# Kernel optimization log

Measured on AMD Instinct MI355X. Metric: run time of the kernel, lower is better.

## Reference

```python
import jax, jax.numpy as jnp
import numpy as np
from jax import lax

D_INNER = 1024
D_STATE = 16
DT_RANK = 32


def conv2d(x, w, b, pad=1):
    y = lax.conv_general_dilated(x, w, (1, 1), [(pad, pad), (pad, pad)],
                                 dimension_numbers=('NCHW', 'OIHW', 'NCHW'))
    return y + b[None, :, None, None]


def maxpool2(x):
    return lax.reduce_window(x, -jnp.inf, lax.max, (1, 1, 2, 2), (1, 1, 2, 2), 'VALID')


def layer_norm(x, w, b, eps=1e-5):
    m = x.mean(-1, keepdims=True)
    v = ((x - m) ** 2).mean(-1, keepdims=True)
    return (x - m) * lax.rsqrt(v + eps) * w + b


def cblock(h, w1, b1, w2, b2):
    return jax.nn.relu(conv2d(jax.nn.relu(conv2d(h, w1, b1)), w2, b2))


def up2(d, w, b):
    # ConvTranspose2d(kernel=2, stride=2): each input pixel -> 2x2 output block
    Bn, Ci, H, W = d.shape
    y = jnp.einsum('bcij,copq->boipjq', d, w).reshape(Bn, w.shape[1], 2 * H, 2 * W)
    return y + b[None, :, None, None]


def eblock(e, d, upw, upb, w1, b1, w2, b2):
    d = up2(d, upw, upb)
    dy = e.shape[2] - d.shape[2]
    dx = e.shape[3] - d.shape[3]
    e = e[:, :, dy // 2:e.shape[2] - dy // 2, dx // 2:e.shape[3] - dx // 2]
    return cblock(jnp.concatenate([e, d], 1), w1, b1, w2, b2)


def mamba(hs, inW, cw, cb, xpW, dtW, dtB, Alog, Dp, outW):
    # standard Mamba-1 mixer: in_proj -> causal depthwise conv -> selective scan -> gate -> out_proj
    Bn, L, _ = hs.shape
    xz = jnp.einsum('bld,ed->ble', hs, inW)                       # [B,L,2*d_inner]
    xi, z = xz[..., :D_INNER], xz[..., D_INNER:]
    xc = lax.conv_general_dilated(xi.transpose(0, 2, 1), cw[:, None, :], (1,), [(3, 0)],
                                  dimension_numbers=('NCH', 'OIH', 'NCH'),
                                  feature_group_count=D_INNER)    # causal, len L
    xc = jax.nn.silu(xc + cb[None, :, None]).transpose(0, 2, 1)   # [B,L,d_inner]
    xdbl = jnp.einsum('bld,ed->ble', xc, xpW)                     # [B,L,dt_rank+2*d_state]
    dt = jax.nn.softplus(jnp.einsum('blr,dr->bld', xdbl[..., :DT_RANK], dtW) + dtB)
    Bs = xdbl[..., DT_RANK:DT_RANK + D_STATE]
    Cs = xdbl[..., DT_RANK + D_STATE:]
    A = -jnp.exp(Alog)                                            # [d_inner,d_state]
    dA = jnp.exp(dt[..., None] * A)                               # [B,L,d_inner,d_state]
    dBu = (dt * xc)[..., None] * Bs[:, :, None, :]

    def step(h, inp):
        dA_t, dBu_t, C_t = inp
        h = dA_t * h + dBu_t
        return h, jnp.einsum('bdn,bn->bd', h, C_t)

    h0 = jnp.zeros((Bn, D_INNER, D_STATE), hs.dtype)
    _, ys = lax.scan(step, h0, (dA.transpose(1, 0, 2, 3), dBu.transpose(1, 0, 2, 3), Cs.transpose(1, 0, 2)))
    y = ys.transpose(1, 0, 2) + Dp * xc
    return jnp.einsum('ble,de->bld', y * jax.nn.silu(z), outW)


def setup_inputs() -> dict:
    key = jax.random.key(0)
    ks = iter(jax.random.split(key, 80))

    def w(shape, fan_in):
        return jax.random.normal(next(ks), shape, jnp.float32) * np.float32(np.sqrt(2.0 / fan_in))

    H = W = 128
    fy = np.fft.fftfreq(H)
    fx = np.fft.fftfreq(W)
    r = np.sqrt(fy[:, None] ** 2 + fx[None, :] ** 2)
    r = r / r.max()
    bands = [(0.0, 0.15), (0.15, 0.35), (0.35, 1.0001)]
    freq_masks = jnp.asarray(np.stack([((r >= lo) & (r < hi)).astype(np.float32) for lo, hi in bands]))

    d = {}
    d['x'] = jax.random.normal(next(ks), (2, 1, H, W), jnp.float32)
    d['freq_masks'] = freq_masks
    for ci, co, n in [(3, 64, 'e1'), (64, 128, 'e2'), (128, 256, 'e3'), (256, 512, 'e4')]:
        d[n + 'w1'] = w((co, ci, 3, 3), ci * 9)
        d[n + 'b1'] = jnp.zeros((co,), jnp.float32)
        d[n + 'w2'] = w((co, co, 3, 3), co * 9)
        d[n + 'b2'] = jnp.zeros((co,), jnp.float32)
    d['cls_token'] = jnp.zeros((1, 1, 512), jnp.float32)
    d['norm_w'] = jnp.ones((24, 512), jnp.float32)
    d['norm_b'] = jnp.zeros((24, 512), jnp.float32)
    d['in_proj_w'] = w((24, 2048, 512), 512)
    d['conv1d_w'] = w((24, 1024, 4), 4)
    d['conv1d_b'] = jnp.zeros((24, 1024), jnp.float32)
    d['x_proj_w'] = w((24, 64, 1024), 1024)
    d['dt_w'] = w((24, 1024, 32), 32)
    d['dt_b'] = jnp.full((24, 1024), float(np.log(np.expm1(0.01))), jnp.float32)
    d['A_log'] = jnp.broadcast_to(jnp.log(jnp.arange(1, 17, dtype=jnp.float32)), (24, 1024, 16)) + 0.0
    d['D_ssm'] = jnp.ones((24, 1024), jnp.float32)
    d['out_proj_w'] = w((24, 512, 1024), 1024)
    for n, ci, co, cc in [('d4', 512, 256, 768), ('d3', 256, 128, 384), ('d2', 128, 64, 192), ('d1', 64, 32, 96)]:
        d[n + 'up_w'] = w((ci, co, 2, 2), ci * 4)
        d[n + 'up_b'] = jnp.zeros((co,), jnp.float32)
        d[n + 'w1'] = w((co, cc, 3, 3), cc * 9)
        d[n + 'b1'] = jnp.zeros((co,), jnp.float32)
        d[n + 'w2'] = w((co, co, 3, 3), co * 9)
        d[n + 'b2'] = jnp.zeros((co,), jnp.float32)
    d['final_w'] = w((4, 32, 1, 1), 32)
    d['final_b'] = jnp.zeros((4,), jnp.float32)
    return d


def reference(x, freq_masks, e1w1, e1b1, e1w2, e1b2, e2w1, e2b1, e2w2, e2b2,
              e3w1, e3b1, e3w2, e3b2, e4w1, e4b1, e4w2, e4b2, cls_token,
              norm_w, norm_b, in_proj_w, conv1d_w, conv1d_b, x_proj_w, dt_w, dt_b,
              A_log, D_ssm, out_proj_w,
              d4up_w, d4up_b, d4w1, d4b1, d4w2, d4b2,
              d3up_w, d3up_b, d3w1, d3b1, d3w2, d3b2,
              d2up_w, d2up_b, d2w1, d2b1, d2w2, d2b2,
              d1up_w, d1up_b, d1w1, d1b1, d1w2, d1b2,
              final_w, final_b):
    # DCT/FFT frequency split: [B,1,H,W] -> [B,3,H,W]
    xf = jnp.fft.fft2(x)
    x_freq = jnp.real(jnp.fft.ifft2(xf * freq_masks[None]))

    e1 = cblock(x_freq, e1w1, e1b1, e1w2, e1b2); p1 = maxpool2(e1)
    e2 = cblock(p1, e2w1, e2b1, e2w2, e2b2); p2 = maxpool2(e2)
    e3 = cblock(p2, e3w1, e3b1, e3w2, e3b2); p3 = maxpool2(e3)
    e4 = cblock(p3, e4w1, e4b1, e4w2, e4b2); p4 = maxpool2(e4)   # [B,512,H/16,W/16]

    Bn, _, Hs, Ws = p4.shape
    seq = p4.reshape(Bn, 512, Hs * Ws).transpose(0, 2, 1)
    tok = jnp.concatenate([jnp.broadcast_to(cls_token, (Bn, 1, 512)), seq], 1)

    params = (norm_w, norm_b, in_proj_w, conv1d_w, conv1d_b, x_proj_w, dt_w, dt_b, A_log, D_ssm, out_proj_w)

    def layer(carry, p):
        hidden, residual = carry
        nw, nb, inW, cw, cb, xpW, dtW, dtB, Alog, Dp, outW = p
        residual = residual + hidden   # first block: residual starts == hidden (faithful)
        hs = layer_norm(residual, nw, nb)
        hs = mamba(hs, inW, cw, cb, xpW, dtW, dtB, Alog, Dp, outW)
        return (hs, residual), None

    (hidden, _), _ = lax.scan(layer, (tok, tok), params)

    xsp = hidden[:, 1:, :].transpose(0, 2, 1).reshape(Bn, 512, Hs, Ws)

    d4 = eblock(e4, xsp, d4up_w, d4up_b, d4w1, d4b1, d4w2, d4b2)
    d3 = eblock(e3, d4, d3up_w, d3up_b, d3w1, d3b1, d3w2, d3b2)
    d2 = eblock(e2, d3, d2up_w, d2up_b, d2w1, d2b1, d2w2, d2b2)
    d1 = eblock(e1, d2, d1up_w, d1up_b, d1w1, d1b1, d1w2, d1b2)

    out = conv2d(d1, final_w, final_b, pad=0)
    out = jax.image.resize(out, (out.shape[0], out.shape[1], out.shape[2] * 16, out.shape[3] * 16), 'bilinear')
    return out
```

## Files before the change

kernel.cpp:

```cpp
#include <hip/hip_runtime.h>
#include <math.h>

#define PI_F 3.14159265358979323846f
typedef _Float16 f16;
typedef __attribute__((ext_vector_type(8))) _Float16 f16x8;
typedef __attribute__((ext_vector_type(4))) float f32x4;

__device__ __forceinline__ float siluf(float x){ return x / (1.f + expf(-x)); }
__device__ __forceinline__ float softplusf(float x){ return fmaxf(x,0.f) + log1pf(expf(-fabsf(x))); }
__device__ __forceinline__ void f2hl(float v, f16& hi, f16& lo){
  hi = (f16)v;
  lo = (f16)(v - (float)hi);
}

__global__ void k_dft_rows(const float* __restrict__ x, float* __restrict__ Tre, float* __restrict__ Tim){
  int v = threadIdx.x; int y = blockIdx.x; int b = blockIdx.y;
  __shared__ float cs[128], sn[128];
  float ang = -2.f*PI_F*(float)v/128.f;
  cs[v]=cosf(ang); sn[v]=sinf(ang);
  __syncthreads();
  const float* row = x + (b*128+y)*128;
  float re=0.f, im=0.f;
  for(int n=0;n<128;n++){ float xv=row[n]; int ph=(v*n)&127; re=fmaf(xv,cs[ph],re); im=fmaf(xv,sn[ph],im); }
  int o=(b*128+y)*128+v; Tre[o]=re; Tim[o]=im;
}
__global__ void k_dft_cols(const float* __restrict__ Tre, const float* __restrict__ Tim,
                           float* __restrict__ Fre, float* __restrict__ Fim){
  int v=threadIdx.x; int u=blockIdx.x; int b=blockIdx.y;
  __shared__ float cs[128], sn[128];
  float ang=-2.f*PI_F*(float)v/128.f; cs[v]=cosf(ang); sn[v]=sinf(ang);
  __syncthreads();
  float re=0.f,im=0.f;
  for(int y=0;y<128;y++){
    int ph=(u*y)&127; float c=cs[ph], s=sn[ph];
    int o=(b*128+y)*128+v;
    float tr=Tre[o], ti=Tim[o];
    re += tr*c - ti*s; im += tr*s + ti*c;
  }
  int o=(b*128+u)*128+v; Fre[o]=re; Fim[o]=im;
}
__global__ void k_idft_cols(const float* __restrict__ Fre,const float* __restrict__ Fim,
                            const float* __restrict__ mask, float* __restrict__ Gre,float* __restrict__ Gim){
  int v=threadIdx.x; int y=blockIdx.x; int m=blockIdx.y; int b=blockIdx.z;
  __shared__ float cs[128], sn[128];
  float ang=-2.f*PI_F*(float)v/128.f; cs[v]=cosf(ang); sn[v]=sinf(ang);
  __syncthreads();
  float re=0.f,im=0.f;
  for(int u=0;u<128;u++){
    int ph=(u*y)&127; float c=cs[ph], s=sn[ph];
    float w = mask[(m*128+u)*128+v];
    int o=(b*128+u)*128+v;
    float fr=Fre[o]*w, fi=Fim[o]*w;
    re += fr*c + fi*s;
    im += fi*c - fr*s;
  }
  int o=((b*3+m)*128+y)*128+v;
  Gre[o]=re*(1.f/128.f); Gim[o]=im*(1.f/128.f);
}
__global__ void k_idft_rows(const float* __restrict__ Gre,const float* __restrict__ Gim, float* __restrict__ xf){
  int xc=threadIdx.x; int y=blockIdx.x; int m=blockIdx.y; int b=blockIdx.z;
  __shared__ float cs[128], sn[128];
  float ang=-2.f*PI_F*(float)xc/128.f; cs[xc]=cosf(ang); sn[xc]=sinf(ang);
  __syncthreads();
  float re=0.f;
  const float* gr=Gre+((b*3+m)*128+y)*128;
  const float* gi=Gim+((b*3+m)*128+y)*128;
  for(int v=0;v<128;v++){
    int ph=(v*xc)&127;
    re += gr[v]*cs[ph] + gi[v]*sn[ph];
  }
  xf[((b*3+m)*128+y)*128+xc] = re*(1.f/128.f);
}

#define NWD 20
struct WAll {
  const float* src[NWD];
  int N[NWD], Kp[NWD], up[NWD], ci[NWD], cip[NWD];
  int cum[NWD+1];
};
__global__ void k_wcvt_all(WAll d, int total, f16* __restrict__ bh, f16* __restrict__ bl){
  int gid = blockIdx.x*256 + threadIdx.x;
  if (gid >= total) return;
  int li = gid; const float* src = d.src[0];
  int N=d.N[0], Kp=d.Kp[0], up=d.up[0], Ci=d.ci[0], cip=d.cip[0];
  #pragma unroll
  for (int j=1;j<NWD;j++){
    if (gid >= d.cum[j]){
      li = gid - d.cum[j]; src=d.src[j]; N=d.N[j];Kp=d.Kp[j];up=d.up[j];Ci=d.ci[j];cip=d.cip[j];
    }
  }
  int n = li / Kp, k = li - n*Kp;
  float v = 0.f;
  if (up){
    int o = n>>2, p=(n>>1)&1, q=n&1;
    if (k < Ci) v = src[(((size_t)k*up + o)*2 + p)*2 + q];
  } else {
    int tap = k / cip, cc = k - tap*cip;
    if (n < N && cc < Ci) v = src[((size_t)n*Ci + cc)*9 + tap];
  }
  f16 h,l; f2hl(v,h,l);
  bh[gid]=h; bl[gid]=l;
}

__global__ void k_im2col(const float* __restrict__ in1, int C1,
                         int H, int W, int wsh, int hwsh, int K, int Kp,
                         f16* __restrict__ Ah, f16* __restrict__ Al){
  int k = blockIdx.x*256 + threadIdx.x;
  int lm = blockIdx.y;
  if (k >= Kp) return;
  float val = 0.f;
  if (k < K){
    int m = lm;
    int b = m >> hwsh;
    int hw = m & ((1<<hwsh)-1);
    int y = hw >> wsh;
    int x = hw & (W-1);
    val = in1[(((size_t)b*C1 + k)*H + y)*W + x];
  }
  f16 h,l; f2hl(val,h,l);
  Ah[(size_t)lm*Kp + k] = h; Al[(size_t)lm*Kp + k] = l;
}

__global__ void k_im2col32(const float* __restrict__ in1, int C1,
                           const float* __restrict__ in2, int C2,
                           int H, int W, int wsh, int hwsh, int K,
                           float* __restrict__ A){
  int k = blockIdx.x*256 + threadIdx.x;
  int m = blockIdx.y;
  if (k >= K) return;
  int ci = k/9; int tt = k - ci*9;
  int dy = tt/3 - 1, dx = tt - (tt/3)*3 - 1;
  int b = m >> hwsh;
  int hw = m & ((1<<hwsh)-1);
  int y = (hw >> wsh) + dy;
  int x = (hw & (W-1)) + dx;
  float val = 0.f;
  if (y >= 0 && y < H && x >= 0 && x < W){
    val = (ci < C1) ? in1[(((size_t)b*C1 + ci)*H + y)*W + x]
                    : in2[(((size_t)b*C2 + (ci-C1))*H + y)*W + x];
  }
  A[(size_t)m*K + k] = val;
}

#define GLLDS(gp, ls) __builtin_amdgcn_global_load_lds( \
    (const __attribute__((address_space(1))) void*)(gp), \
    (__attribute__((address_space(3))) void*)(ls), 16, 0, 0)

template<int NL>
__global__ __launch_bounds__(256) void k_conv_ig(
    const float* __restrict__ in1, int C1, const float* __restrict__ in2, int C2,
    const f16* __restrict__ Wh, const f16* __restrict__ Wl,
    const float* __restrict__ bias, float* __restrict__ out,
    int Co, int H, int W, int wsh, int hwsh, int Cip, int civ)
{
  __shared__ __align__(16) float smI[2*6464];
  __shared__ __align__(16) f16 smW[3*2*2048];
  const int HW = 1<<hwsh;
  const int tw = (W<64)?W:64;
  const int twsh = (wsh<6)?wsh:6;
  const int R = 64>>twsh;
  const int RT = R+2, TWD = tw+2;
  const int nspat = RT*TWD;
  const int CS = ((nspat+3)&~3)+2;
  const int total = nspat*32;
  const int nslab = Cip>>5;
  const int nsteps = 9*nslab;
  const int Kp = 9*Cip;

  int bn = blockIdx.y*64;
  int bm = blockIdx.x*64;
  int t = threadIdx.x;
  int lane = t&63, wv = t>>6;
  int wr = wv>>1, wc = wv&1;

  int b  = bm >> hwsh;
  int hw0 = bm & (HW-1);
  int y0 = hw0 >> wsh;
  int x0 = hw0 & (W-1);

  float bv[2][4];
  {
    int cb = bn + wr*32 + (lane>>4)*4;
    #pragma unroll
    for (int ri=0;ri<2;ri++)
      #pragma unroll
      for (int r=0;r<4;r++){
        int co = cb + ri*16 + r;
        bv[ri][r] = bias[co < Co ? co : Co-1];
      }
    asm volatile("s_waitcnt vmcnt(0)" ::: "memory");
  }

  int goff[NL], loff[NL];
  {
    int ci = 0, s = t;
    if (s >= nspat){ s -= nspat; ci++; }
    if (s >= nspat){ s -= nspat; ci++; }
    #pragma unroll
    for (int j=0;j<NL;j++){
      int rr_=0, sx=s;
      #pragma unroll
      for (int q=0;q<5;q++){ if (sx>=TWD){ sx-=TWD; rr_++; } }
      int gy = y0 - 1 + rr_;
      int gx = x0 - 1 + sx;
      int idx = t + j*256;
      bool intile = (idx < total);
      bool ok = intile && (ci < civ) && (gy>=0) && (gy<H) && (gx>=0) && (gx<W);
      goff[j] = ok ? (ci*HW + gy*W + gx) : -1;
      loff[j] = intile ? (ci*CS + rr_*TWD + sx) : -1;
      s += 256;
      if (s >= nspat){ s -= nspat; ci++; }
      if (s >= nspat){ s -= nspat; ci++; }
      if (s >= nspat){ s -= nspat; ci++; }
    }
  }

  int rr = lane >> 2;
  int cg = (lane & 3) ^ ((lane >> 3) & 3);
  size_t gW = (size_t)(bn + wv*16 + rr)*Kp + cg*8;
  int lb = wv*512;
  auto stage = [&](int bfi, int k0){
    GLLDS(Wh + gW + k0, &smW[(bfi*2+0)*2048 + lb]);
    GLLDS(Wl + gW + k0, &smW[(bfi*2+1)*2048 + lb]);
  };

  int rA = lane & 15, c = lane >> 4;
  int RW = wr*32 + rA; int sW = (RW>>1)&3;
  int offW = RW*32 + 8*(c ^ sW);
  int lp0 = wc*32 + rA, lp1 = lp0 + 16;
  int sid0 = ((lp0>>twsh)+1)*TWD + (lp0 & (tw-1)) + 1;
  int sid1 = ((lp1>>twsh)+1)*TWD + (lp1 & (tw-1)) + 1;
  int cbase = c*8*CS;
  int csj[8];
  #pragma unroll
  for (int j=0;j<8;j++) csj[j] = j*CS;

  auto srcptr = [&](int sl) -> const float* {
    int cbeg = sl*32;
    return (cbeg < C1) ? in1 + ((size_t)(b*C1 + cbeg))*HW
                       : in2 + ((size_t)(b*C2 + (cbeg - C1)))*HW;
  };

  float rin[NL];
  {
    const float* sp = srcptr(0);
    #pragma unroll
    for (int j=0;j<NL;j++) rin[j] = sp[goff[j] < 0 ? 0 : goff[j]];
  }
  stage(0, 0);
  stage(1, Cip);
  stage(2, 2*Cip);
  asm volatile("s_waitcnt vmcnt(6)" ::: "memory");
  #pragma unroll
  for (int j=0;j<NL;j++) if (loff[j] >= 0) smI[loff[j]] = (goff[j] < 0) ? 0.f : rin[j];
  asm volatile("s_waitcnt lgkmcnt(0)" ::: "memory");
  __builtin_amdgcn_s_barrier();
  asm volatile("" ::: "memory");
  if (nslab > 1){
    const float* sp = srcptr(1);
    #pragma unroll
    for (int j=0;j<NL;j++) rin[j] = sp[goff[j] < 0 ? 0 : goff[j]];
  }

  f32x4 zz = {0.f,0.f,0.f,0.f};
  f32x4 acc[2][2];
  acc[0][0]=zz; acc[0][1]=zz; acc[1][0]=zz; acc[1][1]=zz;

  int tcur = 0, scur = 0;
  int stp_t3 = 3, stp_s3 = 0;
  int bfi = 0;

  for (int step = 0; step < nsteps; ++step){
    if (tcur == 0 && step > 0){
      asm volatile("s_waitcnt vmcnt(6)" ::: "memory");
      int wb = (scur & 1)*6464;
      #pragma unroll
      for (int j=0;j<NL;j++) if (loff[j] >= 0) smI[wb + loff[j]] = (goff[j] < 0) ? 0.f : rin[j];
      asm volatile("s_waitcnt lgkmcnt(0)" ::: "memory");
      __builtin_amdgcn_s_barrier();
      asm volatile("" ::: "memory");
      if (scur + 1 < nslab){
        const float* sp = srcptr(scur+1);
        #pragma unroll
        for (int j=0;j<NL;j++) rin[j] = sp[goff[j] < 0 ? 0 : goff[j]];
      }
    }
    if (tcur < 3 && (scur + 1 < nslab)){
      if constexpr (NL == 25) asm volatile("s_waitcnt vmcnt(29)" ::: "memory");
      else if constexpr (NL == 17) asm volatile("s_waitcnt vmcnt(21)" ::: "memory");
      else asm volatile("s_waitcnt vmcnt(18)" ::: "memory");
    } else {
      asm volatile("s_waitcnt vmcnt(4)" ::: "memory");
    }
    __builtin_amdgcn_s_barrier();
    asm volatile("" ::: "memory");

    const f16* bW = &smW[bfi*4096];
    f16x8 w0h = *(const f16x8*)&bW[offW];
    f16x8 w1h = *(const f16x8*)&bW[offW + 512];
    f16x8 w0l = *(const f16x8*)&bW[2048 + offW];
    f16x8 w1l = *(const f16x8*)&bW[2048 + offW + 512];

    int t3v = (tcur >= 6) ? 2 : ((tcur >= 3) ? 1 : 0);
    int doff = (t3v - 1)*TWD + (tcur - 3*t3v) - 1;
    int ib = (scur & 1)*6464 + cbase;
    f16x8 p0h, p0l, p1h, p1l;
    #pragma unroll
    for (int j=0;j<8;j++){
      float v0 = smI[ib + csj[j] + sid0 + doff];
      float v1 = smI[ib + csj[j] + sid1 + doff];
      f16 h0 = (f16)v0; p0h[j] = h0; p0l[j] = (f16)(v0 - (float)h0);
      f16 h1 = (f16)v1; p1h[j] = h1; p1l[j] = (f16)(v1 - (float)h1);
    }
    acc[0][0] = __builtin_amdgcn_mfma_f32_16x16x32_f16(w0h, p0h, acc[0][0], 0,0,0);
    acc[0][1] = __builtin_amdgcn_mfma_f32_16x16x32_f16(w0h, p1h, acc[0][1], 0,0,0);
    acc[1][0] = __builtin_amdgcn_mfma_f32_16x16x32_f16(w1h, p0h, acc[1][0], 0,0,0);
    acc[1][1] = __builtin_amdgcn_mfma_f32_16x16x32_f16(w1h, p1h, acc[1][1], 0,0,0);
    acc[0][0] = __builtin_amdgcn_mfma_f32_16x16x32_f16(w0h, p0l, acc[0][0], 0,0,0);
    acc[0][1] = __builtin_amdgcn_mfma_f32_16x16x32_f16(w0h, p1l, acc[0][1], 0,0,0);
    acc[1][0] = __builtin_amdgcn_mfma_f32_16x16x32_f16(w1h, p0l, acc[1][0], 0,0,0);
    acc[1][1] = __builtin_amdgcn_mfma_f32_16x16x32_f16(w1h, p1l, acc[1][1], 0,0,0);
    acc[0][0] = __builtin_amdgcn_mfma_f32_16x16x32_f16(w0l, p0h, acc[0][0], 0,0,0);
    acc[0][1] = __builtin_amdgcn_mfma_f32_16x16x32_f16(w0l, p1h, acc[0][1], 0,0,0);
    acc[1][0] = __builtin_amdgcn_mfma_f32_16x16x32_f16(w1l, p0h, acc[1][0], 0,0,0);
    acc[1][1] = __builtin_amdgcn_mfma_f32_16x16x32_f16(w1l, p1h, acc[1][1], 0,0,0);

    __builtin_amdgcn_s_barrier();
    asm volatile("" ::: "memory");
    int k0 = (stp_s3 < nslab) ? (stp_t3*Cip + stp_s3*32) : 0;
    stage(bfi, k0);
    if (++stp_t3 == 9){ stp_t3 = 0; stp_s3++; }
    bfi = (bfi == 2) ? 0 : bfi + 1;
    if (++tcur == 9){ tcur = 0; scur++; }
  }

  #pragma unroll
  for (int ri=0;ri<2;ri++)
  #pragma unroll
  for (int fc=0;fc<2;fc++)
  #pragma unroll
  for (int r=0;r<4;r++){
    int co = bn + wr*32 + ri*16 + (lane>>4)*4 + r;
    int pm = bm + wc*32 + fc*16 + (lane&15);
    if (co < Co){
      float v = acc[ri][fc][r] + bv[ri][r];
      v = fmaxf(v, 0.f);
      int hw = pm & (HW-1);
      out[((size_t)b*Co + co)*HW + hw] = v;
    }
  }
}

__global__ void k_creduce(const float* __restrict__ part, const float* __restrict__ bias,
                          float* __restrict__ out, int M, int Np, int msh, int cosh, int hwsh, int S){
  int i = blockIdx.x*256 + threadIdx.x;
  int Co = 1<<cosh;
  if (i >= M*Co) return;
  int co = i >> msh, m = i & (M-1);
  float v = bias[co];
  for (int s=0;s<S;s++) v += part[((size_t)s*M + m)*Np + co];
  v = fmaxf(v, 0.f);
  int HW = 1<<hwsh;
  int b = m >> hwsh, hw = m & (HW-1);
  out[((size_t)b*Co + co)*HW + hw] = v;
}

__global__ __launch_bounds__(256) void k_gemm_hl(
    const f16* __restrict__ Wh, const f16* __restrict__ Wl,
    const f16* __restrict__ Ph, const f16* __restrict__ Pl,
    const float* __restrict__ bias, float* __restrict__ out,
    int N, int Kp, int wsh, int hwsh, int Co)
{
  __shared__ __align__(16) f16 sm[3*4*2048];
  int bn = blockIdx.y*64;
  int bm = blockIdx.x*64;
  int t = threadIdx.x;
  int lane = t & 63, wv = t >> 6;
  int wr = wv >> 1, wc = wv & 1;

  float bv[2][4];
  {
    int cb = bn + wr*32 + (lane>>4)*4;
    #pragma unroll
    for (int ri=0;ri<2;ri++)
      #pragma unroll
      for (int r=0;r<4;r++){
        int co = cb + ri*16 + r;
        int idx = co>>2, lim = N>>2;
// ... 108 lines not shown
  int RP0 = wc*32 + rA;  int swzP = RP0 & 7;
  int cw0 = ((2*c)   ^ swzW)*4;
  int cw1 = ((2*c+1) ^ swzW)*4;
  int pc0 = ((2*c)   ^ swzP)*4;
  int pc1 = ((2*c+1) ^ swzP)*4;

  f32x4 zz = {0.f,0.f,0.f,0.f};
  f32x4 acc[2][2];
  acc[0][0]=zz; acc[0][1]=zz; acc[1][0]=zz; acc[1][1]=zz;

  auto stage = [&](int bfi, int kk){
    GLLDS(Wf + gWoff + kk,                  &smW[bfi*2048 + wv*512]);
    GLLDS(Wf + gWoff + kk + 8*(size_t)ldaW, &smW[bfi*2048 + wv*512 + 256]);
    GLLDS(Pf + gPoff + kk,                  &smP[bfi*2048 + wv*512]);
    GLLDS(Pf + gPoff + kk + 8*(size_t)ldaP, &smP[bfi*2048 + wv*512 + 256]);
  };

  int nt = KS >> 5;
  stage(0, 0);
  stage(1, (nt>1)?32:0);
  stage(2, (nt>2)?64:0);

  for (int tt = 0; tt < nt; ++tt){
    asm volatile("s_waitcnt vmcnt(8)" ::: "memory");
    __builtin_amdgcn_s_barrier();
    asm volatile("" ::: "memory");
    int bfi = tt % 3;
    const float* bW = &smW[bfi*2048];
    const float* bP = &smP[bfi*2048];
    f32x4 a0 = *(const f32x4*)&bW[RW0*32 + cw0];
    f32x4 a1 = *(const f32x4*)&bW[RW0*32 + cw1];
    f32x4 a2 = *(const f32x4*)&bW[RW0*32 + 512 + cw0];
    f32x4 a3 = *(const f32x4*)&bW[RW0*32 + 512 + cw1];
    f32x4 b0 = *(const f32x4*)&bP[RP0*32 + pc0];
    f32x4 b1 = *(const f32x4*)&bP[RP0*32 + pc1];
    f32x4 b2 = *(const f32x4*)&bP[RP0*32 + 512 + pc0];
    f32x4 b3 = *(const f32x4*)&bP[RP0*32 + 512 + pc1];
    f16x8 w0h, w0l, w1h, w1l, p0h, p0l, p1h, p1l;
    #pragma unroll
    for (int j=0;j<4;j++){
      f16 h;
      h=(f16)a0[j]; w0h[j]=h;   w0l[j]  =(f16)(a0[j]-(float)h);
      h=(f16)a1[j]; w0h[4+j]=h; w0l[4+j]=(f16)(a1[j]-(float)h);
      h=(f16)a2[j]; w1h[j]=h;   w1l[j]  =(f16)(a2[j]-(float)h);
      h=(f16)a3[j]; w1h[4+j]=h; w1l[4+j]=(f16)(a3[j]-(float)h);
      h=(f16)b0[j]; p0h[j]=h;   p0l[j]  =(f16)(b0[j]-(float)h);
      h=(f16)b1[j]; p0h[4+j]=h; p0l[4+j]=(f16)(b1[j]-(float)h);
      h=(f16)b2[j]; p1h[j]=h;   p1l[j]  =(f16)(b2[j]-(float)h);
      h=(f16)b3[j]; p1h[4+j]=h; p1l[4+j]=(f16)(b3[j]-(float)h);
    }
    acc[0][0] = __builtin_amdgcn_mfma_f32_16x16x32_f16(w0h, p0h, acc[0][0], 0,0,0);
    acc[0][1] = __builtin_amdgcn_mfma_f32_16x16x32_f16(w0h, p1h, acc[0][1], 0,0,0);
    acc[1][0] = __builtin_amdgcn_mfma_f32_16x16x32_f16(w1h, p0h, acc[1][0], 0,0,0);
    acc[1][1] = __builtin_amdgcn_mfma_f32_16x16x32_f16(w1h, p1h, acc[1][1], 0,0,0);
    acc[0][0] = __builtin_amdgcn_mfma_f32_16x16x32_f16(w0h, p0l, acc[0][0], 0,0,0);
    acc[0][1] = __builtin_amdgcn_mfma_f32_16x16x32_f16(w0h, p1l, acc[0][1], 0,0,0);
    acc[1][0] = __builtin_amdgcn_mfma_f32_16x16x32_f16(w1h, p0l, acc[1][0], 0,0,0);
    acc[1][1] = __builtin_amdgcn_mfma_f32_16x16x32_f16(w1h, p1l, acc[1][1], 0,0,0);
    acc[0][0] = __builtin_amdgcn_mfma_f32_16x16x32_f16(w0l, p0h, acc[0][0], 0,0,0);
    acc[0][1] = __builtin_amdgcn_mfma_f32_16x16x32_f16(w0l, p1h, acc[0][1], 0,0,0);
    acc[1][0] = __builtin_amdgcn_mfma_f32_16x16x32_f16(w1l, p0h, acc[1][0], 0,0,0);
    acc[1][1] = __builtin_amdgcn_mfma_f32_16x16x32_f16(w1l, p1h, acc[1][1], 0,0,0);
    __builtin_amdgcn_s_barrier();
    asm volatile("" ::: "memory");
    int kn = (tt+3 < nt) ? (tt+3)*32 : 0;
    stage(bfi, kn);
  }

  #pragma unroll
  for (int ri=0;ri<2;ri++)
  #pragma unroll
  for (int fc=0;fc<2;fc++)
  #pragma unroll
  for (int r=0;r<4;r++){
    int co = bn + wr*32 + ri*16 + (lane>>4)*4 + r;
    int m  = bm + wc*32 + fc*16 + (lane&15);
    if (m < Mreal)
      out[((size_t)blockIdx.z*sliceStride + m)*ldc + co] = acc[ri][fc][r];
  }
}

__global__ __launch_bounds__(256) void k_dt(
    const float* __restrict__ xdp, const float* __restrict__ dtW,
    const float* __restrict__ dtB, float* __restrict__ dtb)
{
  __shared__ float smP[64*36];
  __shared__ float smW[64*36];
  int bn = blockIdx.x*64;
  int bm = blockIdx.y*64;
  int t = threadIdx.x, lane = t&63, wv = t>>6, wr = wv>>1, wc = wv&1;
  {
    int row = t>>2, c0 = (t&3)*8;
    #pragma unroll
    for (int j=0;j<8;j++){
      int cc = c0+j;
      float pv = 0.f;
      #pragma unroll
      for (int s=0;s<4;s++) pv += xdp[((size_t)(s*192) + bm+row)*64 + cc];
      smP[row*36 + cc] = pv;
      smW[row*36 + cc] = dtW[(size_t)(bn+row)*32 + cc];
    }
  }
  __syncthreads();
  int rA = lane&15, c = lane>>4;
  int c8 = c*8;
  f32x4 a0 = *(const f32x4*)&smW[(wr*32+rA)*36 + c8];
  f32x4 a1 = *(const f32x4*)&smW[(wr*32+rA)*36 + c8+4];
  f32x4 a2 = *(const f32x4*)&smW[(wr*32+16+rA)*36 + c8];
  f32x4 a3 = *(const f32x4*)&smW[(wr*32+16+rA)*36 + c8+4];
  f32x4 b0 = *(const f32x4*)&smP[(wc*32+rA)*36 + c8];
  f32x4 b1 = *(const f32x4*)&smP[(wc*32+rA)*36 + c8+4];
  f32x4 b2 = *(const f32x4*)&smP[(wc*32+16+rA)*36 + c8];
  f32x4 b3 = *(const f32x4*)&smP[(wc*32+16+rA)*36 + c8+4];
  f16x8 w0h, w0l, w1h, w1l, p0h, p0l, p1h, p1l;
  #pragma unroll
  for (int j=0;j<4;j++){
    f16 h;
    h=(f16)a0[j]; w0h[j]=h;   w0l[j]  =(f16)(a0[j]-(float)h);
    h=(f16)a1[j]; w0h[4+j]=h; w0l[4+j]=(f16)(a1[j]-(float)h);
    h=(f16)a2[j]; w1h[j]=h;   w1l[j]  =(f16)(a2[j]-(float)h);
    h=(f16)a3[j]; w1h[4+j]=h; w1l[4+j]=(f16)(a3[j]-(float)h);
    h=(f16)b0[j]; p0h[j]=h;   p0l[j]  =(f16)(b0[j]-(float)h);
    h=(f16)b1[j]; p0h[4+j]=h; p0l[4+j]=(f16)(b1[j]-(float)h);
    h=(f16)b2[j]; p1h[j]=h;   p1l[j]  =(f16)(b2[j]-(float)h);
    h=(f16)b3[j]; p1h[4+j]=h; p1l[4+j]=(f16)(b3[j]-(float)h);
  }
  f32x4 zz = {0.f,0.f,0.f,0.f};
  f32x4 acc[2][2];
  acc[0][0]=zz; acc[0][1]=zz; acc[1][0]=zz; acc[1][1]=zz;
  acc[0][0] = __builtin_amdgcn_mfma_f32_16x16x32_f16(w0h, p0h, acc[0][0], 0,0,0);
  acc[0][1] = __builtin_amdgcn_mfma_f32_16x16x32_f16(w0h, p1h, acc[0][1], 0,0,0);
  acc[1][0] = __builtin_amdgcn_mfma_f32_16x16x32_f16(w1h, p0h, acc[1][0], 0,0,0);
  acc[1][1] = __builtin_amdgcn_mfma_f32_16x16x32_f16(w1h, p1h, acc[1][1], 0,0,0);
  acc[0][0] = __builtin_amdgcn_mfma_f32_16x16x32_f16(w0h, p0l, acc[0][0], 0,0,0);
  acc[0][1] = __builtin_amdgcn_mfma_f32_16x16x32_f16(w0h, p1l, acc[0][1], 0,0,0);
  acc[1][0] = __builtin_amdgcn_mfma_f32_16x16x32_f16(w1h, p0l, acc[1][0], 0,0,0);
  acc[1][1] = __builtin_amdgcn_mfma_f32_16x16x32_f16(w1h, p1l, acc[1][1], 0,0,0);
  acc[0][0] = __builtin_amdgcn_mfma_f32_16x16x32_f16(w0l, p0h, acc[0][0], 0,0,0);
  acc[0][1] = __builtin_amdgcn_mfma_f32_16x16x32_f16(w0l, p1h, acc[0][1], 0,0,0);
  acc[1][0] = __builtin_amdgcn_mfma_f32_16x16x32_f16(w1l, p0h, acc[1][0], 0,0,0);
  acc[1][1] = __builtin_amdgcn_mfma_f32_16x16x32_f16(w1l, p1h, acc[1][1], 0,0,0);
  #pragma unroll
  for (int ri=0;ri<2;ri++)
  #pragma unroll
  for (int fc=0;fc<2;fc++)
  #pragma unroll
  for (int r=0;r<4;r++){
    int co = bn + wr*32 + ri*16 + (lane>>4)*4 + r;
    int m  = bm + wc*32 + fc*16 + (lane&15);
    if (m < 130)
      dtb[(size_t)m*1024 + co] = softplusf(acc[ri][fc][r] + dtB[co]);
  }
}

__global__ void k_maxpool2(const float* __restrict__ in, float* __restrict__ out, int BC, int H, int W){
  int Ho=H/2, Wo=W/2;
  int idx = blockIdx.x*blockDim.x + threadIdx.x;
  if (idx >= BC*Ho*Wo) return;
  int xo = idx % Wo; int yo = (idx / Wo) % Ho; int c = idx / (Wo*Ho);
  const float* p = in + ((size_t)c*H + 2*yo)*W + 2*xo;
  out[idx] = fmaxf(fmaxf(p[0],p[1]), fmaxf(p[W],p[W+1]));
}

__global__ void k_build_tok(const float* __restrict__ p4, const float* __restrict__ cls,
                            float* __restrict__ hidp, float* __restrict__ residual){
  int idx = blockIdx.x*blockDim.x+threadIdx.x;
  if (idx >= 2*65*512) return;
  int d = idx % 512; int l = (idx/512)%65; int b = idx/(512*65);
  float v = (l==0) ? cls[d] : p4[((size_t)b*512+d)*64 + (l-1)];
  int row = b*65 + l;
  residual[(size_t)row*512 + d] = v;
  hidp[(size_t)row*512 + d] = v;
  #pragma unroll
  for (int s=1;s<8;s++) hidp[((size_t)(s*192) + row)*512 + d] = 0.f;
}

__global__ void k_add_ln(float* __restrict__ residual, const float* __restrict__ hidp,
                         const float* __restrict__ nw, const float* __restrict__ nb,
                         float* __restrict__ hs){
  int row = blockIdx.x;
  int t = threadIdx.x;
  __shared__ float red[256];
  size_t base = (size_t)row*512;
  float h0 = 0.f, h1 = 0.f;
  #pragma unroll
  for (int s=0;s<8;s++){
    h0 += hidp[((size_t)(s*192) + row)*512 + t];
    h1 += hidp[((size_t)(s*192) + row)*512 + 256 + t];
  }
  float v0 = residual[base + t]       + h0;
  float v1 = residual[base + 256 + t] + h1;
  residual[base+t]=v0; residual[base+256+t]=v1;
  red[t]=v0+v1; __syncthreads();
  for(int o=128;o>0;o>>=1){ if(t<o) red[t]+=red[t+o]; __syncthreads(); }
  float mean = red[0]/512.f; __syncthreads();
  float d0=v0-mean, d1=v1-mean;
  red[t]=d0*d0+d1*d1; __syncthreads();
  for(int o=128;o>0;o>>=1){ if(t<o) red[t]+=red[t+o]; __syncthreads(); }
  float rstd = rsqrtf(red[0]/512.f + 1e-5f);
  hs[base+t]     = d0*rstd*nw[t]     + nb[t];
  hs[base+256+t] = d1*rstd*nw[256+t] + nb[256+t];
}

__global__ void k_conv1d_silu(const float* __restrict__ xzp, const float* __restrict__ cw,
                              const float* __restrict__ cb, float* __restrict__ xc){
  int d = blockIdx.x*blockDim.x + threadIdx.x;
  int l = blockIdx.y, b = blockIdx.z;
  if (d>=1024) return;
  float acc = cb[d];
  #pragma unroll
  for(int k=0;k<4;k++){
    int lp = l-3+k;
    if (lp>=0){
      size_t r = (size_t)(b*65+lp);
      float xzv = xzp[r*2048 + d] + xzp[(r + 192)*2048 + d];
      acc = fmaf(xzv, cw[d*4+k], acc);
    }
  }
  xc[((size_t)(b*65+l))*1024 + d] = siluf(acc);
}

__global__ void k_scan(const float* __restrict__ dt, const float* __restrict__ xc,
                       const float* __restrict__ xdp, const float* __restrict__ xzp,
                       const float* __restrict__ Alog, const float* __restrict__ Dp,
                       float* __restrict__ gt){
  int gid = blockIdx.x*blockDim.x + threadIdx.x;
  if (gid >= 2*1024*16) return;
  int n = gid & 15;
  int d = (gid >> 4) & 1023;
  int b = gid >> 14;
  float A = -expf(Alog[d*16+n]);
  float Dv = Dp[d];
  float h = 0.f;
  for (int l=0;l<65;l++){
    size_t r = (size_t)(b*65+l);
    float dtv = dt[r*1024+d];
    float xcv = xc[r*1024+d];
    float Bn = 0.f, Cn = 0.f;
    #pragma unroll
    for (int s=0;s<4;s++){
      Bn += xdp[((size_t)(s*192) + r)*64 + 32 + n];
      Cn += xdp[((size_t)(s*192) + r)*64 + 48 + n];
    }
    h = fmaf(expf(dtv*A), h, dtv*xcv*Bn);
    float y = h*Cn;
    y += __shfl_xor(y, 1); y += __shfl_xor(y, 2);
    y += __shfl_xor(y, 4); y += __shfl_xor(y, 8);
    if (n==0){
      float zv = xzp[r*2048 + 1024 + d] + xzp[(r + 192)*2048 + 1024 + d];
      gt[r*1024+d] = (y + Dv*xcv) * siluf(zv);
    }
  }
}

__global__ void k_xsp(const float* __restrict__ hidp, float* __restrict__ xsp){
  int idx = blockIdx.x*blockDim.x+threadIdx.x;
  if (idx>=2*512*64) return;
  int j = idx & 63; int c = (idx>>6)&511; int b = idx>>15;
  int row = b*65 + 1 + j;
  float v = 0.f;
  #pragma unroll
  for (int s=0;s<8;s++) v += hidp[((size_t)(s*192) + row)*512 + c];
  xsp[idx] = v;
}

__global__ void k_conv1x1(const float* __restrict__ in, const float* __restrict__ w,
                          const float* __restrict__ bias, float* __restrict__ out){
  int hw = blockIdx.x*blockDim.x+threadIdx.x; if (hw>=128*128) return;
  int o = blockIdx.y, b = blockIdx.z;
  float acc = bias[o];
  #pragma unroll
  for(int c=0;c<32;c++) acc = fmaf(in[((size_t)(b*32+c))*16384 + hw], w[o*32+c], acc);
  out[((size_t)(b*4+o))*16384 + hw] = acc;
}

__global__ void k_resize16(const float* __restrict__ in, float* __restrict__ out){
  size_t idx = (size_t)blockIdx.x*blockDim.x + threadIdx.x;
  if (idx >= (size_t)2*4*2048*2048) return;
  int x = idx & 2047; int y = (int)((idx>>11)&2047); int c = (int)(idx>>22);
  float sx = ((float)x+0.5f)*(1.f/16.f) - 0.5f;
  float sy = ((float)y+0.5f)*(1.f/16.f) - 0.5f;
  int x0 = (int)floorf(sx); float fx = sx-(float)x0;
  int y0 = (int)floorf(sy); float fy = sy-(float)y0;
  int x0c = max(x0,0), x1c = min(x0+1,127);
  int y0c = max(y0,0), y1c = min(y0+1,127);
  const float* p = in + (size_t)c*16384;
  float v00=p[y0c*128+x0c], v01=p[y0c*128+x1c], v10=p[y1c*128+x0c], v11=p[y1c*128+x1c];
  out[idx] = (1.f-fy)*((1.f-fx)*v00 + fx*v01) + fy*((1.f-fx)*v10 + fx*v11);
}

#define MAX_A_ELEMS 524288

extern "C" void kernel_launch(void* const* d_in, const int* in_sizes, int n_in,
                              void* d_out, int out_size, void* d_ws, size_t ws_size,
                              hipStream_t stream) {
  const float* x        = (const float*)d_in[0];
  const float* masks    = (const float*)d_in[1];
  const float* ew1[4] = {(const float*)d_in[2],(const float*)d_in[6],(const float*)d_in[10],(const float*)d_in[14]};
  const float* eb1[4] = {(const float*)d_in[3],(const float*)d_in[7],(const float*)d_in[11],(const float*)d_in[15]};
  const float* ew2[4] = {(const float*)d_in[4],(const float*)d_in[8],(const float*)d_in[12],(const float*)d_in[16]};
  const float* eb2[4] = {(const float*)d_in[5],(const float*)d_in[9],(const float*)d_in[13],(const float*)d_in[17]};
  const float* cls      = (const float*)d_in[18];
  const float* norm_w   = (const float*)d_in[19];
  const float* norm_b   = (const float*)d_in[20];
  const float* in_proj  = (const float*)d_in[21];
  const float* conv1d_w = (const float*)d_in[22];
  const float* conv1d_b = (const float*)d_in[23];
  const float* x_proj   = (const float*)d_in[24];
  const float* dt_w     = (const float*)d_in[25];
  const float* dt_b     = (const float*)d_in[26];
  const float* A_log    = (const float*)d_in[27];
  const float* D_ssm    = (const float*)d_in[28];
  const float* out_proj = (const float*)d_in[29];
  const float* dup_w[4] = {(const float*)d_in[30],(const float*)d_in[36],(const float*)d_in[42],(const float*)d_in[48]};
  const float* dup_b[4] = {(const float*)d_in[31],(const float*)d_in[37],(const float*)d_in[43],(const float*)d_in[49]};
  const float* dw1[4]   = {(const float*)d_in[32],(const float*)d_in[38],(const float*)d_in[44],(const float*)d_in[50]};
  const float* db1[4]   = {(const float*)d_in[33],(const float*)d_in[39],(const float*)d_in[45],(const float*)d_in[51]};
  const float* dw2[4]   = {(const float*)d_in[34],(const float*)d_in[40],(const float*)d_in[46],(const float*)d_in[52]};
  const float* db2[4]   = {(const float*)d_in[35],(const float*)d_in[41],(const float*)d_in[47],(const float*)d_in[53]};
  const float* final_w  = (const float*)d_in[54];
  const float* final_b  = (const float*)d_in[55];
  float* out = (float*)d_out;

  float* W = (float*)d_ws;
  size_t off = 0;
  auto alloc = [&](size_t n){ float* p = W + off; off += n; return p; };

  float* Tre = alloc(32768);  float* Tim = alloc(32768);
  float* Fre = alloc(32768);  float* Fim = alloc(32768);
  float* Gre = alloc(196608); float* Gim = alloc(196608);
  float* xfreq = alloc(98304);
  float* tmpA = alloc(2097152);
  float* e1 = alloc(2097152);
  float* p1 = alloc(524288);
  float* e2 = alloc(1048576);
  float* p2 = alloc(262144);
  float* e3 = alloc(524288);
  float* p3 = alloc(131072);
  float* e4 = alloc(262144);
  float* p4 = alloc(65536);
  float* residual = alloc(66560);
  float* xsp = alloc(65536);
  float* tmpB = alloc(1048576);
  float* d4 = alloc(131072);
  float* d3 = alloc(262144);
  float* d2 = alloc(524288);
  float* d1 = alloc(1048576);
  float* fin = alloc(131072);
  (void)ws_size; (void)n_in; (void)in_sizes; (void)out_size;

  WAll wa;
  {
    const float* s[NWD] = { ew1[0], ew2[0], ew1[1], ew2[1], ew1[2], ew2[2], ew1[3], ew2[3],
                            dw1[0], dw2[0], dw1[1], dw2[1], dw1[2], dw2[2], dw1[3], dw2[3],
                            dup_w[0], dup_w[1], dup_w[2], dup_w[3] };
    const int N_[NWD]  = {64,64,128,128,256,256,512,512, 256,256,128,128,64,64,32,32, 1024,512,256,128};
    const int CI_[NWD] = {3,64,64,128,128,256,256,512, 768,256,384,128,192,64,96,32, 512,256,128,64};
    const int U_[NWD]  = {0,0,0,0,0,0,0,0, 0,0,0,0,0,0,0,0, 256,128,64,32};
    int cacc = 0;
    for (int i=0;i<NWD;i++){
      wa.src[i]=s[i]; wa.N[i]=N_[i]; wa.up[i]=U_[i]; wa.ci[i]=CI_[i];
      int cip = (CI_[i]+31)&~31;
      wa.cip[i] = cip;
      wa.Kp[i] = U_[i] ? CI_[i] : 9*cip;
      wa.cum[i]=cacc;
      int Np=(N_[i]+63)&~63;
      cacc += Np*wa.Kp[i];
    }
    wa.cum[NWD]=cacc;
  }
  int wtotal = wa.cum[NWD];

  f16* q = (f16*)d_out;
  f16* Ahi = q; q += MAX_A_ELEMS;
  f16* Alo = q; q += MAX_A_ELEMS;
  f16* Ball_h = q; q += wtotal;
  f16* Ball_l = q; q += wtotal;
  float* fb = (float*)q;
  size_t foff = 0;
  auto falloc = [&](size_t n){ float* p = fb + foff; foff += n; return p; };
  float* convpart = falloc(2097152);
  float* Af32 = falloc(7340032);
  float* xzp  = falloc(2*192*2048);
  float* xdp  = falloc(4*192*64);
  float* hidp = falloc(8*192*512);
  float* hs   = falloc(192*512);
  float* xc   = falloc(192*1024);
  float* gt   = falloc(192*1024);
  float* dtb  = falloc(192*1024);

  hipLaunchKernelGGL(k_wcvt_all, dim3((wtotal+255)/256), dim3(256), 0, stream, wa, wtotal, Ball_h, Ball_l);

  hipLaunchKernelGGL(k_dft_rows, dim3(128,2), dim3(128), 0, stream, x, Tre, Tim);
  hipLaunchKernelGGL(k_dft_cols, dim3(128,2), dim3(128), 0, stream, Tre, Tim, Fre, Fim);
  hipLaunchKernelGGL(k_idft_cols, dim3(128,3,2), dim3(128), 0, stream, Fre, Fim, masks, Gre, Gim);
  hipLaunchKernelGGL(k_idft_rows, dim3(128,3,2), dim3(128), 0, stream, Gre, Gim, xfreq);

  auto ctz = [](int v){ int s=0; while(!(v&1)){v>>=1;s++;} return s; };
  auto conv_ig = [&](const float* i1,int C1,const float* i2,int C2,
                     int widx, const float* bias, float* o, int Co, int H){
    int Wd = H;
    int Ci = C1+C2, Cip = (Ci+31)&~31;
    int M = 2*H*Wd, Np = (Co+63)&~63;
    int wsh = ctz(Wd), hwsh = ctz(H*Wd);
    int civ = Ci < 32 ? Ci : 32;
    const f16* bh = Ball_h + wa.cum[widx];
    const f16* bl = Ball_l + wa.cum[widx];
    dim3 g(M/64, Np/64);
    if (Wd >= 64)
      hipLaunchKernelGGL((k_conv_ig<25>), g, dim3(256), 0, stream, i1,C1,i2,C2,bh,bl,bias,o,Co,H,Wd,wsh,hwsh,Cip,civ);
    else if (Wd == 32)
      hipLaunchKernelGGL((k_conv_ig<17>), g, dim3(256), 0, stream, i1,C1,i2,C2,bh,bl,bias,o,Co,H,Wd,wsh,hwsh,Cip,civ);
    else
      hipLaunchKernelGGL((k_conv_ig<14>), g, dim3(256), 0, stream, i1,C1,i2,C2,bh,bl,bias,o,Co,H,Wd,wsh,hwsh,Cip,civ);
  };
  auto conv_sk = [&](const float* i1,int C1,const float* i2,int C2,
                     const float* wraw, const float* bias, float* o, int Co, int H, int S){
    int Wd = H;
    int Ci = C1+C2, K = Ci*9;
    int M = 2*H*Wd;
    int wsh = ctz(Wd), hwsh = ctz(H*Wd);
    hipLaunchKernelGGL(k_im2col32, dim3((K+255)/256, M), dim3(256), 0, stream,
                       i1, C1, i2, C2, H, Wd, wsh, hwsh, K, Af32);
    int KS = K / S;
    hipLaunchKernelGGL(k_gemm_w32s, dim3(M/64, Co/64, S), dim3(256), 0, stream,
                       wraw, K, Af32, K, convpart, Co, KS, M, Co, M);
    hipLaunchKernelGGL(k_creduce, dim3((M*Co+255)/256), dim3(256), 0, stream,
                       convpart, bias, o, M, Co, ctz(M), ctz(Co), hwsh, S);
  };
  auto up_bf = [&](const float* in, int widx, const float* bias, float* o,
                   int Ci,int Co,int Hi){
    int Kp=Ci, N=4*Co;
    int M=2*Hi*Hi;
    int wsh=ctz(Hi), hwsh=ctz(Hi*Hi);
    const f16* bh = Ball_h + wa.cum[widx];
    const f16* bl = Ball_l + wa.cum[widx];
    hipLaunchKernelGGL(k_im2col, dim3((Kp+255)/256, M), dim3(256), 0, stream,
                       in, Ci, Hi, Hi, wsh, hwsh, Ci, Kp, Ahi, Alo);
    hipLaunchKernelGGL(k_gemm_hl, dim3(M/64, N/64), dim3(256), 0, stream,
                       bh, bl, Ahi, Alo, bias, o, N, Kp, wsh, hwsh, Co);
  };

  conv_ig(xfreq,3,  nullptr,0, 0, eb1[0], tmpA, 64, 128);
  conv_ig(tmpA,64,  nullptr,0, 1, eb2[0], e1,   64, 128);
  hipLaunchKernelGGL(k_maxpool2, dim3((2*64*64*64+255)/256), dim3(256), 0, stream, e1, p1, 2*64, 128,128);
  conv_ig(p1,64,    nullptr,0, 2, eb1[1], tmpA, 128, 64);
  conv_ig(tmpA,128, nullptr,0, 3, eb2[1], e2,   128, 64);
  hipLaunchKernelGGL(k_maxpool2, dim3((2*128*32*32+255)/256), dim3(256), 0, stream, e2, p2, 2*128, 64,64);
  conv_sk(p2,128,   nullptr,0, ew1[2], eb1[2], tmpA, 256, 32, 4);
  conv_sk(tmpA,256, nullptr,0, ew2[2], eb2[2], e3,   256, 32, 4);
  hipLaunchKernelGGL(k_maxpool2, dim3((2*256*16*16+255)/256), dim3(256), 0, stream, e3, p3, 2*256, 32,32);
  conv_sk(p3,256,   nullptr,0, ew1[3], eb1[3], tmpA, 512, 16, 8);
  conv_sk(tmpA,512, nullptr,0, ew2[3], eb2[3], e4,   512, 16, 8);
  hipLaunchKernelGGL(k_maxpool2, dim3((2*512*8*8+255)/256), dim3(256), 0, stream, e4, p4, 2*512, 16,16);

  hipLaunchKernelGGL(k_build_tok, dim3((2*65*512+255)/256), dim3(256), 0, stream, p4, cls, hidp, residual);
  for (int l=0;l<24;l++){
    const float* nw   = norm_w   + (size_t)l*512;
    const float* nb   = norm_b   + (size_t)l*512;
    const float* inW  = in_proj  + (size_t)l*2048*512;
    const float* cw   = conv1d_w + (size_t)l*1024*4;
    const float* cb   = conv1d_b + (size_t)l*1024;
    const float* xpW  = x_proj   + (size_t)l*64*1024;
    const float* dtW  = dt_w     + (size_t)l*1024*32;
    const float* dtB  = dt_b     + (size_t)l*1024;
    const float* Alg  = A_log    + (size_t)l*1024*16;
    const float* Dp   = D_ssm    + (size_t)l*1024;
    const float* outW = out_proj + (size_t)l*512*1024;

    hipLaunchKernelGGL(k_add_ln, dim3(130), dim3(256), 0, stream, residual, hidp, nw, nb, hs);
    hipLaunchKernelGGL(k_gemm_w32s, dim3(3,32,2), dim3(256), 0, stream,
                       inW, 512, hs, 512, xzp, 2048, 256, 130, 2048, 192);
    hipLaunchKernelGGL(k_conv1d_silu, dim3(4,65,2), dim3(256), 0, stream, xzp, cw, cb, xc);
    hipLaunchKernelGGL(k_gemm_w32s, dim3(3,1,4), dim3(256), 0, stream,
                       xpW, 1024, xc, 1024, xdp, 64, 256, 130, 64, 192);
    hipLaunchKernelGGL(k_dt, dim3(16,3), dim3(256), 0, stream, xdp, dtW, dtB, dtb);
    hipLaunchKernelGGL(k_scan, dim3(128), dim3(256), 0, stream, dtb, xc, xdp, xzp, Alg, Dp, gt);
    hipLaunchKernelGGL(k_gemm_w32s, dim3(3,8,8), dim3(256), 0, stream,
                       outW, 1024, gt, 1024, hidp, 512, 128, 130, 512, 192);
  }
  hipLaunchKernelGGL(k_xsp, dim3((2*512*64+255)/256), dim3(256), 0, stream, hidp, xsp);

  up_bf(xsp, 16, dup_b[0], tmpB, 512, 256, 8);
  conv_sk(e4,512, tmpB,256, dw1[0], db1[0], tmpA, 256, 16, 8);
  conv_sk(tmpA,256, nullptr,0, dw2[0], db2[0], d4, 256, 16, 8);
  up_bf(d4, 17, dup_b[1], tmpB, 256, 128, 16);
  conv_sk(e3,256, tmpB,128, dw1[1], db1[1], tmpA, 128, 32, 4);
  conv_sk(tmpA,128, nullptr,0, dw2[1], db2[1], d3, 128, 32, 4);
  up_bf(d3, 18, dup_b[2], tmpB, 128, 64, 32);
  conv_ig(e2,128, tmpB,64, 12, db1[2], tmpA, 64, 64);
  conv_ig(tmpA,64, nullptr,0, 13, db2[2], d2, 64, 64);
  up_bf(d2, 19, dup_b[3], tmpB, 64, 32, 64);
  conv_ig(e1,64, tmpB,32, 14, db1[3], tmpA, 32, 128);
  conv_ig(tmpA,32, nullptr,0, 15, db2[3], d1, 32, 128);

  hipLaunchKernelGGL(k_conv1x1, dim3((16384+255)/256, 4, 2), dim3(256), 0, stream, d1, final_w, final_b, fin);
  hipLaunchKernelGGL(k_resize16, dim3((size_t)(2*4*2048*2048)/256), dim3(256), 0, stream, fin, out);
}
```

Baseline: 3.120 ms.

## Trim unused weight conversions, single-buffer conv input, precompute reduced x_proj

Weight conversion now covers only the 12 weights the fp16 paths actually use, dropping the conversions for layers handled by other kernels. The implicit-GEMM conv input tile in shared memory goes from double to single buffered, which halves its footprint, presumably to fit more blocks per CU. k_dt also writes the split-K-reduced x_proj output once so the scan reads it directly instead of summing four partials per element. Single buffering is risky: the prefetch write into smI after the barrier can overwrite data other waves are still reading unless the existing barriers already order it.

```diff
diff --git a/kernel.cpp b/kernel.cpp
--- a/kernel.cpp
+++ b/kernel.cpp
@@ -72,7 +72,7 @@
   xf[((b*3+m)*128+y)*128+xc] = re*(1.f/128.f);
 }
 
-#define NWD 20
+#define NWD 12
 struct WAll {
   const float* src[NWD];
   int N[NWD], Kp[NWD], up[NWD], ci[NWD], cip[NWD];
@@ -153,7 +153,7 @@
     const float* __restrict__ bias, float* __restrict__ out,
     int Co, int H, int W, int wsh, int hwsh, int Cip, int civ)
 {
-  __shared__ __align__(16) float smI[2*6464];
+  __shared__ __align__(16) float smI[6464];
   __shared__ __align__(16) f16 smW[3*2*2048];
   const int HW = 1<<hwsh;
   const int tw = (W<64)?W:64;
@@ -273,9 +273,8 @@
   for (int step = 0; step < nsteps; ++step){
     if (tcur == 0 && step > 0){
       asm volatile("s_waitcnt vmcnt(6)" ::: "memory");
-      int wb = (scur & 1)*6464;
       #pragma unroll
-      for (int j=0;j<NL;j++) if (loff[j] >= 0) smI[wb + loff[j]] = (goff[j] < 0) ? 0.f : rin[j];
+      for (int j=0;j<NL;j++) if (loff[j] >= 0) smI[loff[j]] = (goff[j] < 0) ? 0.f : rin[j];
       asm volatile("s_waitcnt lgkmcnt(0)" ::: "memory");
       __builtin_amdgcn_s_barrier();
       asm volatile("" ::: "memory");
@@ -303,7 +302,7 @@
 
     int t3v = (tcur >= 6) ? 2 : ((tcur >= 3) ? 1 : 0);
     int doff = (t3v - 1)*TWD + (tcur - 3*t3v) - 1;
-    int ib = (scur & 1)*6464 + cbase;
+    int ib = cbase;
     f16x8 p0h, p0l, p1h, p1l;
     #pragma unroll
     for (int j=0;j<8;j++){
@@ -578,22 +577,28 @@
 
 __global__ __launch_bounds__(256) void k_dt(
     const float* __restrict__ xdp, const float* __restrict__ dtW,
-    const float* __restrict__ dtB, float* __restrict__ dtb)
+    const float* __restrict__ dtB, float* __restrict__ dtb, float* __restrict__ xds)
 {
-  __shared__ float smP[64*36];
+  __shared__ float smP[64*68];
   __shared__ float smW[64*36];
   int bn = blockIdx.x*64;
   int bm = blockIdx.y*64;
   int t = threadIdx.x, lane = t&63, wv = t>>6, wr = wv>>1, wc = wv&1;
   {
-    int row = t>>2, c0 = (t&3)*8;
+    int row = t>>2, c0 = (t&3)*16;
     #pragma unroll
-    for (int j=0;j<8;j++){
+    for (int j=0;j<16;j++){
       int cc = c0+j;
       float pv = 0.f;
       #pragma unroll
       for (int s=0;s<4;s++) pv += xdp[((size_t)(s*192) + bm+row)*64 + cc];
-      smP[row*36 + cc] = pv;
+      smP[row*68 + cc] = pv;
+      if (blockIdx.x == 0) xds[(size_t)(bm+row)*64 + cc] = pv;
+    }
+    int cw0 = (t&3)*8;
+    #pragma unroll
+    for (int j=0;j<8;j++){
+      int cc = cw0+j;
       smW[row*36 + cc] = dtW[(size_t)(bn+row)*32 + cc];
     }
   }
@@ -604,10 +609,10 @@
   f32x4 a1 = *(const f32x4*)&smW[(wr*32+rA)*36 + c8+4];
   f32x4 a2 = *(const f32x4*)&smW[(wr*32+16+rA)*36 + c8];
   f32x4 a3 = *(const f32x4*)&smW[(wr*32+16+rA)*36 + c8+4];
-  f32x4 b0 = *(const f32x4*)&smP[(wc*32+rA)*36 + c8];
-  f32x4 b1 = *(const f32x4*)&smP[(wc*32+rA)*36 + c8+4];
-  f32x4 b2 = *(const f32x4*)&smP[(wc*32+16+rA)*36 + c8];
-  f32x4 b3 = *(const f32x4*)&smP[(wc*32+16+rA)*36 + c8+4];
+  f32x4 b0 = *(const f32x4*)&smP[(wc*32+rA)*68 + c8];
+  f32x4 b1 = *(const f32x4*)&smP[(wc*32+rA)*68 + c8+4];
+  f32x4 b2 = *(const f32x4*)&smP[(wc*32+16+rA)*68 + c8];
+  f32x4 b3 = *(const f32x4*)&smP[(wc*32+16+rA)*68 + c8+4];
   f16x8 w0h, w0l, w1h, w1l, p0h, p0l, p1h, p1l;
   #pragma unroll
   for (int j=0;j<4;j++){
@@ -717,7 +722,7 @@
 }
 
 __global__ void k_scan(const float* __restrict__ dt, const float* __restrict__ xc,
-                       const float* __restrict__ xdp, const float* __restrict__ xzp,
+                       const float* __restrict__ xds, const float* __restrict__ xzp,
                        const float* __restrict__ Alog, const float* __restrict__ Dp,
                        float* __restrict__ gt){
   int gid = blockIdx.x*blockDim.x + threadIdx.x;
@@ -732,12 +737,8 @@
     size_t r = (size_t)(b*65+l);
     float dtv = dt[r*1024+d];
     float xcv = xc[r*1024+d];
-    float Bn = 0.f, Cn = 0.f;
-    #pragma unroll
-    for (int s=0;s<4;s++){
-      Bn += xdp[((size_t)(s*192) + r)*64 + 32 + n];
-      Cn += xdp[((size_t)(s*192) + r)*64 + 48 + n];
-    }
+    float Bn = xds[r*64 + 32 + n];
+    float Cn = xds[r*64 + 48 + n];
     h = fmaf(expf(dtv*A), h, dtv*xcv*Bn);
     float y = h*Cn;
     y += __shfl_xor(y, 1); y += __shfl_xor(y, 2);
@@ -847,12 +848,12 @@
 
   WAll wa;
   {
-    const float* s[NWD] = { ew1[0], ew2[0], ew1[1], ew2[1], ew1[2], ew2[2], ew1[3], ew2[3],
-                            dw1[0], dw2[0], dw1[1], dw2[1], dw1[2], dw2[2], dw1[3], dw2[3],
+    const float* s[NWD] = { ew1[0], ew2[0], ew1[1], ew2[1],
+                            dw1[2], dw2[2], dw1[3], dw2[3],
                             dup_w[0], dup_w[1], dup_w[2], dup_w[3] };
-    const int N_[NWD]  = {64,64,128,128,256,256,512,512, 256,256,128,128,64,64,32,32, 1024,512,256,128};
-    const int CI_[NWD] = {3,64,64,128,128,256,256,512, 768,256,384,128,192,64,96,32, 512,256,128,64};
-    const int U_[NWD]  = {0,0,0,0,0,0,0,0, 0,0,0,0,0,0,0,0, 256,128,64,32};
+    const int N_[NWD]  = {64,64,128,128, 64,64,32,32, 1024,512,256,128};
+    const int CI_[NWD] = {3,64,64,128, 192,64,96,32, 512,256,128,64};
+    const int U_[NWD]  = {0,0,0,0, 0,0,0,0, 256,128,64,32};
     int cacc = 0;
     for (int i=0;i<NWD;i++){
       wa.src[i]=s[i]; wa.N[i]=N_[i]; wa.up[i]=U_[i]; wa.ci[i]=CI_[i];
@@ -879,6 +880,7 @@
   float* Af32 = falloc(7340032);
   float* xzp  = falloc(2*192*2048);
   float* xdp  = falloc(4*192*64);
+  float* xds  = falloc(192*64);
   float* hidp = falloc(8*192*512);
   float* hs   = falloc(192*512);
   float* xc   = falloc(192*1024);
@@ -970,25 +972,25 @@
     hipLaunchKernelGGL(k_conv1d_silu, dim3(4,65,2), dim3(256), 0, stream, xzp, cw, cb, xc);
     hipLaunchKernelGGL(k_gemm_w32s, dim3(3,1,4), dim3(256), 0, stream,
                        xpW, 1024, xc, 1024, xdp, 64, 256, 130, 64, 192);
-    hipLaunchKernelGGL(k_dt, dim3(16,3), dim3(256), 0, stream, xdp, dtW, dtB, dtb);
-    hipLaunchKernelGGL(k_scan, dim3(128), dim3(256), 0, stream, dtb, xc, xdp, xzp, Alg, Dp, gt);
+    hipLaunchKernelGGL(k_dt, dim3(16,3), dim3(256), 0, stream, xdp, dtW, dtB, dtb, xds);
+    hipLaunchKernelGGL(k_scan, dim3(128), dim3(256), 0, stream, dtb, xc, xds, xzp, Alg, Dp, gt);
     hipLaunchKernelGGL(k_gemm_w32s, dim3(3,8,8), dim3(256), 0, stream,
                        outW, 1024, gt, 1024, hidp, 512, 128, 130, 512, 192);
   }
   hipLaunchKernelGGL(k_xsp, dim3((2*512*64+255)/256), dim3(256), 0, stream, hidp, xsp);
 
-  up_bf(xsp, 16, dup_b[0], tmpB, 512, 256, 8);
+  up_bf(xsp, 8, dup_b[0], tmpB, 512, 256, 8);
   conv_sk(e4,512, tmpB,256, dw1[0], db1[0], tmpA, 256, 16, 8);
   conv_sk(tmpA,256, nullptr,0, dw2[0], db2[0], d4, 256, 16, 8);
-  up_bf(d4, 17, dup_b[1], tmpB, 256, 128, 16);
+  up_bf(d4, 9, dup_b[1], tmpB, 256, 128, 16);
   conv_sk(e3,256, tmpB,128, dw1[1], db1[1], tmpA, 128, 32, 4);
   conv_sk(tmpA,128, nullptr,0, dw2[1], db2[1], d3, 128, 32, 4);
-  up_bf(d3, 18, dup_b[2], tmpB, 128, 64, 32);
-  conv_ig(e2,128, tmpB,64, 12, db1[2], tmpA, 64, 64);
-  conv_ig(tmpA,64, nullptr,0, 13, db2[2], d2, 64, 64);
-  up_bf(d2, 19, dup_b[3], tmpB, 64, 32, 64);
-  conv_ig(e1,64, tmpB,32, 14, db1[3], tmpA, 32, 128);
-  conv_ig(tmpA,32, nullptr,0, 15, db2[3], d1, 32, 128);
+  up_bf(d3, 10, dup_b[2], tmpB, 128, 64, 32);
+  conv_ig(e2,128, tmpB,64, 4, db1[2], tmpA, 64, 64);
+  conv_ig(tmpA,64, nullptr,0, 5, db2[2], d2, 64, 64);
+  up_bf(d2, 11, dup_b[3], tmpB, 64, 32, 64);
+  conv_ig(e1,64, tmpB,32, 6, db1[3], tmpA, 32, 128);
+  conv_ig(tmpA,32, nullptr,0, 7, db2[3], d1, 32, 128);
 
   hipLaunchKernelGGL(k_conv1x1, dim3((16384+255)/256, 4, 2), dim3(256), 0, stream, d1, final_w, final_b, fin);
   hipLaunchKernelGGL(k_resize16, dim3((size_t)(2*4*2048*2048)/256), dim3(256), 0, stream, fin, out);
```

After: 3.268 ms. 4.7% more time.
